# Kernel tuning notes

Measured on AMD Instinct MI355X. Metric: run time of the kernel, lower is better.

Reference implementation:

```python
import jax, jax.numpy as jnp
import numpy as np

B, S, E, H = 4, 2048, 1024, 16
D = E // H


def setup_inputs() -> dict:
    key = jax.random.key(0)
    ks = jax.random.split(key, 4)
    scale = 0.02
    x = jax.random.normal(ks[0], (B, S, E), dtype=jnp.float32)
    in_proj_w = jax.random.normal(ks[1], (3 * E, E), dtype=jnp.float32) * scale
    in_proj_b = jnp.zeros((3 * E,), dtype=jnp.float32)
    out_w = jax.random.normal(ks[2], (E, E), dtype=jnp.float32) * scale
    out_b = jnp.zeros((E,), dtype=jnp.float32)
    rel_bias = jax.random.normal(ks[3], (2 * 32 + 1, H), dtype=jnp.float32) * 0.02
    return {"x": x, "in_proj_w": in_proj_w, "in_proj_b": in_proj_b,
            "out_w": out_w, "out_b": out_b, "rel_bias": rel_bias,
            "max_rel_dist": 32}


def reference(x, in_proj_w, in_proj_b, out_w, out_b, rel_bias, max_rel_dist):
    b, s, e = x.shape
    h = rel_bias.shape[1]
    d = e // h
    # relative-position indices, clamped: [S, S]
    i = jnp.arange(s)[:, None]
    j = jnp.arange(s)[None, :]
    rel = jnp.clip(i - j, -max_rel_dist, max_rel_dist) + max_rel_dist
    # gather per-pair per-head bias then average over heads -> single 2D mask
    attn_mask = jnp.mean(rel_bias[rel], axis=-1)  # [S, S]
    # fused QKV projection (PyTorch in_proj: x @ W^T + b)
    qkv = x @ in_proj_w.T + in_proj_b           # [B, S, 3E]
    q, k, v = jnp.split(qkv, 3, axis=-1)
    q = q.reshape(b, s, h, d)
    k = k.reshape(b, s, h, d)
    v = v.reshape(b, s, h, d)
    scale = 1.0 / jnp.sqrt(jnp.asarray(d, dtype=x.dtype))
    scores = jnp.einsum('bqhd,bkhd->bhqk', q, k) * scale + attn_mask  # [B,H,S,S]
    probs = jax.nn.softmax(scores, axis=-1)
    ctx = jnp.einsum('bhqk,bkhd->bqhd', probs, v).reshape(b, s, e)
    return ctx @ out_w.T + out_b
```

## Files before the change

kernel.cpp:

```cpp
#include <hip/hip_runtime.h>
#include <math.h>

#define B_ 4
#define S_ 2048
#define E_ 1024
#define H_ 16
#define D_ 64
#define MRD 32

typedef __bf16 bf16x8 __attribute__((ext_vector_type(8)));
typedef float f32x4 __attribute__((ext_vector_type(4)));
typedef unsigned short us8 __attribute__((ext_vector_type(8)));
typedef unsigned short us4 __attribute__((ext_vector_type(4)));

union frag_cvt { us8 u; bf16x8 b; };
union h_cvt { __bf16 h; unsigned short u; };

__device__ __forceinline__ unsigned short bhi(float x) {
    h_cvt c; c.h = (__bf16)x; return c.u;
}
__device__ __forceinline__ float bf16_f(unsigned short h) {
    union { unsigned int u; float f; } c;
    c.u = ((unsigned int)h) << 16;
    return c.f;
}

__device__ __forceinline__ void async_copy16(const void* g, void* l) {
    __builtin_amdgcn_global_load_lds(
        (const __attribute__((address_space(1))) void*)g,
        (__attribute__((address_space(3))) void*)l,
        16, 0, 0);
}

__device__ __forceinline__ f32x4 mf16(const frag_cvt& a, const frag_cvt& b, f32x4 c) {
    return __builtin_amdgcn_mfma_f32_16x16x32_bf16(a.b, b.b, c, 0, 0, 0);
}

#define QSCL 0.18033688f
#define L2E  1.44269504f

#define SBAR0() __builtin_amdgcn_sched_barrier(0)

__global__ __launch_bounds__(128) void cvt_bf16(
    const float* __restrict__ in, unsigned short* __restrict__ out, int K)
{
    const int r  = blockIdx.x;
    const int k8 = threadIdx.x * 8;
    if (k8 >= K) return;
    const float* p = in + (size_t)r * K + k8;
    float4 a = *(const float4*)p;
    float4 b = *(const float4*)(p + 4);
    float xs[8] = {a.x, a.y, a.z, a.w, b.x, b.y, b.z, b.w};
    us8 hu;
#pragma unroll
    for (int j = 0; j < 8; ++j) hu[j] = bhi(xs[j]);
    *(us8*)&out[(size_t)r * K + k8] = hu;
}

__global__ __launch_bounds__(128) void split_hilo(
    const float* __restrict__ in, unsigned short* __restrict__ out, int K)
{
    const int r  = blockIdx.x;
    const int k8 = threadIdx.x * 8;
    if (k8 >= K) return;
    const float* p = in + (size_t)r * K + k8;
    float4 a = *(const float4*)p;
    float4 b = *(const float4*)(p + 4);
    float xs[8] = {a.x, a.y, a.z, a.w, b.x, b.y, b.z, b.w};
    us8 hu, lu;
#pragma unroll
    for (int j = 0; j < 8; ++j) {
        unsigned short hb = bhi(xs[j]);
        hu[j] = hb;
        lu[j] = bhi(xs[j] - bf16_f(hb));
    }
    *(us8*)&out[(size_t)r * 2 * K + k8]     = hu;
    *(us8*)&out[(size_t)r * 2 * K + K + k8] = lu;
}

__device__ __forceinline__ void stage_unit(const unsigned short* g, int grs,
                                           unsigned short* lu, int t)
{
#pragma unroll
    for (int l = 0; l < 2; ++l) {
        const int f  = l * 512 + t;
        const int ri = f >> 3;
        const int cs = ((f & 7) ^ (ri & 7)) * 8;
        async_copy16(g + (size_t)ri * grs + cs,
                     lu + l * 4096 + (t >> 6) * 512);
    }
}

template<int MODE>
__global__ __launch_bounds__(512, 2) void gemm8(
    const unsigned short* __restrict__ Ag, const unsigned short* __restrict__ Bg,
    const float* __restrict__ bias,
    unsigned short* __restrict__ O0, unsigned short* __restrict__ O1,
    unsigned short* __restrict__ O2, float* __restrict__ Cf)
{
    constexpr int KD = (MODE == 0) ? 1024 : 3072;
    constexpr int NT = KD / 64;
    constexpr int AS = (MODE == 0) ? 1024 : 2048;
    constexpr int BS = (MODE == 0) ? 1024 : 2048;

    __shared__ unsigned short sbuf[2][24576];

    const int t    = threadIdx.x;
    const int lane = t & 63;
    const int w    = t >> 6;
    const int ln   = lane & 15;
    const int quad = lane >> 4;
    const int wm   = w >> 1;
    const int wn   = w & 1;
    const int m0   = blockIdx.x * 256;
    const int n0   = blockIdx.y * 128;

    auto mapA = [](int kk) -> int {
        return (MODE == 0) ? kk : (kk < 1024 ? kk : kk - 1024);
    };
    auto mapB = [](int kk) -> int {
        return (MODE == 0) ? kk : (kk < 2048 ? kk : kk - 2048);
    };

    const int swz = (ln & 7) << 3;
    const int kq0 = (quad * 8) ^ swz;
    const int kq1 = (32 + quad * 8) ^ swz;

    f32x4 acc[4][4];
#pragma unroll
    for (int i = 0; i < 4; ++i)
#pragma unroll
        for (int j = 0; j < 4; ++j)
            acc[i][j] = (f32x4){0.f, 0.f, 0.f, 0.f};

    stage_unit(Ag + (size_t)m0 * AS + mapA(0),         AS, &sbuf[0][0],     t);
    stage_unit(Ag + (size_t)(m0 + 128) * AS + mapA(0), AS, &sbuf[0][8192],  t);
    stage_unit(Bg + (size_t)n0 * BS + mapB(0),         BS, &sbuf[0][16384], t);
    stage_unit(Bg + (size_t)n0 * BS + mapB(64),        BS, &sbuf[1][16384], t);
    stage_unit(Ag + (size_t)m0 * AS + mapA(64),        AS, &sbuf[1][0],     t);
    asm volatile("s_waitcnt vmcnt(4)" ::: "memory");
    SBAR0();
    __builtin_amdgcn_s_barrier();
    SBAR0();

    for (int k = 0; k < NT; ++k) {
        unsigned short* bufc = sbuf[k & 1];
        unsigned short* bufn = sbuf[(k & 1) ^ 1];
        frag_cvt a0[2][2], a1[2][2], b0[2][2], b1[2][2];

#pragma unroll
        for (int i = 0; i < 2; ++i) {
            const int ra = (wm * 64 + i * 16 + ln) * 64;
            a0[i][0].u = *(const us8*)&bufc[ra + kq0];
            a0[i][1].u = *(const us8*)&bufc[ra + kq1];
            const int rb = 16384 + (wn * 64 + i * 16 + ln) * 64;
            b0[i][0].u = *(const us8*)&bufc[rb + kq0];
            b0[i][1].u = *(const us8*)&bufc[rb + kq1];
        }
        if (k + 1 < NT)
            stage_unit(Ag + (size_t)(m0 + 128) * AS + mapA((k + 1) * 64),
                       AS, &bufn[8192], t);
        SBAR0(); __builtin_amdgcn_s_barrier(); SBAR0();
        __builtin_amdgcn_s_setprio(1);
#pragma unroll
        for (int i = 0; i < 2; ++i)
#pragma unroll
            for (int j = 0; j < 2; ++j) {
                acc[i][j] = mf16(a0[i][0], b0[j][0], acc[i][j]);
                acc[i][j] = mf16(a0[i][1], b0[j][1], acc[i][j]);
            }
        __builtin_amdgcn_s_setprio(0);
        SBAR0(); __builtin_amdgcn_s_barrier(); SBAR0();

#pragma unroll
        for (int i = 0; i < 2; ++i) {
            const int rb = 16384 + (wn * 64 + (i + 2) * 16 + ln) * 64;
            b1[i][0].u = *(const us8*)&bufc[rb + kq0];
            b1[i][1].u = *(const us8*)&bufc[rb + kq1];
        }
        SBAR0(); __builtin_amdgcn_s_barrier(); SBAR0();
        __builtin_amdgcn_s_setprio(1);
#pragma unroll
        for (int i = 0; i < 2; ++i)
#pragma unroll
            for (int j = 0; j < 2; ++j) {
                acc[i][j + 2] = mf16(a0[i][0], b1[j][0], acc[i][j + 2]);
                acc[i][j + 2] = mf16(a0[i][1], b1[j][1], acc[i][j + 2]);
            }
        __builtin_amdgcn_s_setprio(0);
        SBAR0(); __builtin_amdgcn_s_barrier(); SBAR0();

#pragma unroll
        for (int i = 0; i < 2; ++i) {
            const int ra = (wm * 64 + (i + 2) * 16 + ln) * 64;
            a1[i][0].u = *(const us8*)&bufc[ra + kq0];
            a1[i][1].u = *(const us8*)&bufc[ra + kq1];
        }
        if (k + 2 < NT)
            stage_unit(Bg + (size_t)n0 * BS + mapB((k + 2) * 64),
                       BS, &bufc[16384], t);
        SBAR0(); __builtin_amdgcn_s_barrier(); SBAR0();
        __builtin_amdgcn_s_setprio(1);
#pragma unroll
        for (int i = 0; i < 2; ++i)
#pragma unroll
            for (int j = 0; j < 2; ++j) {
                acc[i + 2][j + 2] = mf16(a1[i][0], b1[j][0], acc[i + 2][j + 2]);
                acc[i + 2][j + 2] = mf16(a1[i][1], b1[j][1], acc[i + 2][j + 2]);
            }
        __builtin_amdgcn_s_setprio(0);
        SBAR0(); __builtin_amdgcn_s_barrier(); SBAR0();

        if (k + 2 < NT)
            stage_unit(Ag + (size_t)m0 * AS + mapA((k + 2) * 64),
                       AS, &bufc[0], t);
        SBAR0(); __builtin_amdgcn_s_barrier(); SBAR0();
        __builtin_amdgcn_s_setprio(1);
#pragma unroll
        for (int i = 0; i < 2; ++i)
#pragma unroll
            for (int j = 0; j < 2; ++j) {
                acc[i + 2][j] = mf16(a1[i][0], b0[j][0], acc[i + 2][j]);
                acc[i + 2][j] = mf16(a1[i][1], b0[j][1], acc[i + 2][j]);
            }
        __builtin_amdgcn_s_setprio(0);
        if (k + 2 < NT) {
            asm volatile("s_waitcnt vmcnt(4)" ::: "memory");
        } else if (k + 1 < NT) {
            asm volatile("s_waitcnt vmcnt(0)" ::: "memory");
        }
        SBAR0(); __builtin_amdgcn_s_barrier(); SBAR0();
    }

    if constexpr (MODE == 0) {
        if (n0 < E_) {
#pragma unroll
            for (int j = 0; j < 4; ++j) {
                const int col = n0 + wn * 64 + j * 16 + ln;
                const float bv = bias[col];
                const int h = (col & (E_ - 1)) >> 6, d = col & 63;
#pragma unroll
                for (int i = 0; i < 4; ++i) {
#pragma unroll
                    for (int r = 0; r < 4; ++r) {
                        const int row = m0 + wm * 64 + i * 16 + quad * 4 + r;
                        const int b = row >> 11, s = row & (S_ - 1);
                        O0[((size_t)(b * 16 + h) * S_ + s) * 64 + d] =
                            bhi((acc[i][j][r] + bv) * QSCL);
                    }
                }
            }
        } else if (n0 < 2 * E_) {
#pragma unroll
            for (int j = 0; j < 4; ++j) {
                const int col = n0 + wn * 64 + j * 16 + ln;
                const float bv = bias[col];
                const int h = (col & (E_ - 1)) >> 6, d = col & 63;
#pragma unroll
                for (int i = 0; i < 4; ++i) {
#pragma unroll
                    for (int r = 0; r < 4; ++r) {
                        const int row = m0 + wm * 64 + i * 16 + quad * 4 + r;
                        const int b = row >> 11, s = row & (S_ - 1);
                        O1[((size_t)(b * 16 + h) * S_ + s) * 64 +
                           (((d >> 3) ^ (s & 7)) * 8) + (d & 7)] =
                            bhi(acc[i][j][r] + bv);
                    }
                }
            }
        } else {
#pragma unroll
            for (int j = 0; j < 4; ++j) {
                const int col = n0 + wn * 64 + j * 16 + ln;
                const float bv = bias[col];
                const int h = (col & (E_ - 1)) >> 6, d = col & 63;
#pragma unroll
                for (int i = 0; i < 4; ++i) {
                    const int row0 = m0 + wm * 64 + i * 16 + quad * 4;
                    const int b = row0 >> 11, s0 = row0 & (S_ - 1);
                    const int tile = s0 >> 6;
                    const int g = (s0 >> 3) & 7;
                    us4 o;
#pragma unroll
                    for (int r = 0; r < 4; ++r) o[r] = bhi(acc[i][j][r] + bv);
                    *(us4*)&O2[(size_t)(b * 16 + h) * S_ * 64 + tile * 4096 +
                               d * 64 + ((g ^ (d & 7)) * 8) + (quad & 1) * 4] = o;
                }
            }
        }
    } else {
#pragma unroll
        for (int j = 0; j < 4; ++j) {
            const int col = n0 + wn * 64 + j * 16 + ln;
            const float bv = bias[col];
#pragma unroll
            for (int i = 0; i < 4; ++i) {
                const int row = m0 + wm * 64 + i * 16 + quad * 4;
#pragma unroll
                for (int r = 0; r < 4; ++r)
                    Cf[(size_t)(row + r) * E_ + col] = acc[i][j][r] + bv;
            }
        }
    }
}

__global__ __launch_bounds__(256, 4) void attn_mfma5(
    const unsigned short* __restrict__ Qb, const unsigned short* __restrict__ K2,
    const unsigned short* __restrict__ Vt2, const float* __restrict__ rel_bias,
    unsigned short* __restrict__ ctx2)
{
    __shared__ unsigned short Kt[64 * 64];
    __shared__ unsigned short Vt[64 * 64];
    __shared__ unsigned short Pt[128 * 72];
    __shared__ float bias_s[65];

    const int t    = threadIdx.x;
    const int w    = t >> 6;
    const int lane = t & 63;
    const int ln   = lane & 15;
    const int quad = lane >> 4;

    const int bh = blockIdx.x;
    const int b  = bh >> 4;
    const int h  = bh & 15;
    const int q0 = blockIdx.y * 128;

    if (t < 65) {
        float s = 0.f;
#pragma unroll
        for (int hh = 0; hh < 16; ++hh) s += rel_bias[t * 16 + hh];
        bias_s[t] = s * (L2E / 16.f);
    }

    frag_cvt qf[2][2];
#pragma unroll
    for (int mf = 0; mf < 2; ++mf) {
        const unsigned short* qp =
            Qb + ((size_t)bh * S_ + q0 + w * 32 + mf * 16 + ln) * 64;
        qf[mf][0].u = *(const us8*)(qp + quad * 8);
        qf[mf][1].u = *(const us8*)(qp + 32 + quad * 8);
    }

    frag_cvt ones;
#pragma unroll
    for (int j = 0; j < 8; ++j) ones.u[j] = 0x3F80;

    f32x4 O[2][4];
#pragma unroll
    for (int mf = 0; mf < 2; ++mf)
#pragma unroll
        for (int n = 0; n < 4; ++n) O[mf][n] = (f32x4){0.f, 0.f, 0.f, 0.f};
    f32x4 lacc[2] = {(f32x4){0.f, 0.f, 0.f, 0.f}, (f32x4){0.f, 0.f, 0.f, 0.f}};

    const unsigned short* Kg = K2  + (size_t)bh * S_ * 64;
    const unsigned short* Vg = Vt2 + (size_t)bh * S_ * 64;

    for (int k0 = 0; k0 < S_; k0 += 64) {
        __syncthreads();
        {
            const unsigned short* kg = Kg + (size_t)k0 * 64;
            const unsigned short* vg = Vg + (size_t)k0 * 64;
            const int uo = w * 512;
            async_copy16(kg + uo + lane * 8,        &Kt[uo]);
            async_copy16(kg + 2048 + uo + lane * 8, &Kt[2048 + uo]);
            async_copy16(vg + uo + lane * 8,        &Vt[uo]);
            async_copy16(vg + 2048 + uo + lane * 8, &Vt[2048 + uo]);
        }
        __syncthreads();

        f32x4 sa[2][4];
#pragma unroll
        for (int n = 0; n < 4; ++n) {
            sa[0][n] = (f32x4){0.f, 0.f, 0.f, 0.f};
            sa[1][n] = (f32x4){0.f, 0.f, 0.f, 0.f};
            const int ro = (n * 16 + ln) * 64;
#pragma unroll
            for (int ks = 0; ks < 2; ++ks) {
                frag_cvt kh;
                kh.u = *(const us8*)&Kt[ro + (((ks * 4 + quad) ^ (ln & 7)) * 8)];
                sa[0][n] = __builtin_amdgcn_mfma_f32_16x16x32_bf16(
                    qf[0][ks].b, kh.b, sa[0][n], 0, 0, 0);
                sa[1][n] = __builtin_amdgcn_mfma_f32_16x16x32_bf16(
                    qf[1][ks].b, kh.b, sa[1][n], 0, 0, 0);
            }
        }

        const bool inband = (k0 >= q0 - 64) && (k0 <= q0 + 128);
        float cb = 0.f;
        if (!inband) cb = bias_s[(k0 < q0) ? 64 : 0];
#pragma unroll
        for (int mf = 0; mf < 2; ++mf) {
#pragma unroll
            for (int n = 0; n < 4; ++n) {
#pragma unroll
                for (int r = 0; r < 4; ++r) {
                    float s2;
                    if (inband) {
                        const int q   = q0 + w * 32 + mf * 16 + quad * 4 + r;
                        const int key = k0 + n * 16 + ln;
                        int rel = q - key;
                        rel = (rel < -MRD) ? -MRD : (rel > MRD ? MRD : rel);
                        s2 = sa[mf][n][r] + bias_s[rel + MRD];
                    } else {
                        s2 = sa[mf][n][r] + cb;
                    }
                    const int qrow = w * 32 + mf * 16 + quad * 4 + r;
                    const int pos = (n * 16 + ln) ^ ((qrow & 8) << 1);
                    Pt[qrow * 72 + pos] = bhi(__builtin_amdgcn_exp2f(s2));
                }
            }
        }

#pragma unroll
        for (int ks = 0; ks < 2; ++ks) {
            frag_cvt pa[2];
#pragma unroll
            for (int mf = 0; mf < 2; ++mf) {
                const int prow = w * 32 + mf * 16 + ln;
                pa[mf].u = *(const us8*)&Pt[prow * 72 +
                           ((ks * 32 + quad * 8) ^ ((prow & 8) << 1))];
                lacc[mf] = __builtin_amdgcn_mfma_f32_16x16x32_bf16(
                    pa[mf].b, ones.b, lacc[mf], 0, 0, 0);
            }
#pragma unroll
            for (int n = 0; n < 4; ++n) {
                frag_cvt vh;
                vh.u = *(const us8*)&Vt[(n * 16 + ln) * 64 +
                                        (((ks * 4 + quad) ^ (ln & 7)) * 8)];
                O[0][n] = __builtin_amdgcn_mfma_f32_16x16x32_bf16(
                    pa[0].b, vh.b, O[0][n], 0, 0, 0);
                O[1][n] = __builtin_amdgcn_mfma_f32_16x16x32_bf16(
                    pa[1].b, vh.b, O[1][n], 0, 0, 0);
            }
        }
    }

#pragma unroll
    for (int mf = 0; mf < 2; ++mf) {
        float inv[4];
#pragma unroll
        for (int r = 0; r < 4; ++r) inv[r] = 1.f / lacc[mf][r];
#pragma unroll
        for (int n = 0; n < 4; ++n) {
            const int k = h * D_ + n * 16 + ln;
#pragma unroll
            for (int r = 0; r < 4; ++r) {
                const int q = q0 + w * 32 + mf * 16 + quad * 4 + r;
                const float v = O[mf][n][r] * inv[r];
                unsigned short hb = bhi(v);
                const size_t rb = (size_t)(b * S_ + q) * (2 * E_);
                ctx2[rb + k]      = hb;
                ctx2[rb + E_ + k] = bhi(v - bf16_f(hb));
            }
        }
    }
}

extern "C" void kernel_launch(void* const* d_in, const int* in_sizes, int n_in,
                              void* d_out, int out_size, void* d_ws, size_t ws_size,
                              hipStream_t stream)
{
    const float* x         = (const float*)d_in[0];
    const float* in_proj_w = (const float*)d_in[1];
    const float* in_proj_b = (const float*)d_in[2];
    const float* out_w     = (const float*)d_in[3];
    const float* out_b     = (const float*)d_in[4];
    const float* rel_bias  = (const float*)d_in[5];
    float* out = (float*)d_out;

    const int M = B_ * S_;
    const size_t PH = (size_t)B_ * H_ * S_ * 64;

    unsigned short* Qb   = (unsigned short*)d_ws;
    unsigned short* K2   = Qb + PH;
    unsigned short* Vt2  = K2 + PH;
    unsigned short* W2o  = Vt2 + PH;
    unsigned short* Wqkv = W2o + (size_t)E_ * 2 * E_;
    unsigned short* A2c  = Wqkv + (size_t)3 * E_ * E_;
    unsigned short* Axb  = A2c;

    cvt_bf16<<<M,      128, 0, stream>>>(x,         Axb,  E_);
    cvt_bf16<<<3 * E_, 128, 0, stream>>>(in_proj_w, Wqkv, E_);

    {
        dim3 grid(M / 256, (3 * E_) / 128);
        gemm8<0><<<grid, 512, 0, stream>>>(Axb, Wqkv, in_proj_b,
                                           Qb, K2, Vt2, nullptr);
    }
    {
        dim3 grid(B_ * H_, S_ / 128);
        attn_mfma5<<<grid, 256, 0, stream>>>(Qb, K2, Vt2, rel_bias, A2c);
    }
    split_hilo<<<E_, 128, 0, stream>>>(out_w, W2o, E_);
    {
        dim3 grid(M / 256, E_ / 128);
        gemm8<1><<<grid, 512, 0, stream>>>(A2c, W2o, out_b,
                                           nullptr, nullptr, nullptr, out);
    }
}
```

Before: 332.3 us.

## Simplify GEMM main loop to single load-then-compute phase per k-tile

Replaces the four-phase interleaved GEMM loop, which used many barriers, sched_barriers and staggered per-unit async stages, with a simpler schedule. Each k-step now loads all A/B fragments from LDS, runs all 32 MFMAs, then issues the full next-next tile prefetch between two barriers. This cuts barrier count and scheduling constraints, but loses fine-grained overlap of the LDS reads and global loads with MFMA work, and raises register pressure from holding all fragments at once.

```diff
diff --git a/kernel.cpp b/kernel.cpp
--- a/kernel.cpp
+++ b/kernel.cpp
@@ -38,8 +38,6 @@
 
 #define QSCL 0.18033688f
 #define L2E  1.44269504f
-
-#define SBAR0() __builtin_amdgcn_sched_barrier(0)
 
 __global__ __launch_bounds__(128) void cvt_bf16(
     const float* __restrict__ in, unsigned short* __restrict__ out, int K)
@@ -133,103 +131,53 @@
         for (int j = 0; j < 4; ++j)
             acc[i][j] = (f32x4){0.f, 0.f, 0.f, 0.f};
 
-    stage_unit(Ag + (size_t)m0 * AS + mapA(0),         AS, &sbuf[0][0],     t);
-    stage_unit(Ag + (size_t)(m0 + 128) * AS + mapA(0), AS, &sbuf[0][8192],  t);
-    stage_unit(Bg + (size_t)n0 * BS + mapB(0),         BS, &sbuf[0][16384], t);
-    stage_unit(Bg + (size_t)n0 * BS + mapB(64),        BS, &sbuf[1][16384], t);
-    stage_unit(Ag + (size_t)m0 * AS + mapA(64),        AS, &sbuf[1][0],     t);
-    asm volatile("s_waitcnt vmcnt(4)" ::: "memory");
-    SBAR0();
+    stage_unit(Ag + (size_t)m0 * AS + mapA(0),          AS, &sbuf[0][0],     t);
+    stage_unit(Ag + (size_t)(m0 + 128) * AS + mapA(0),  AS, &sbuf[0][8192],  t);
+    stage_unit(Bg + (size_t)n0 * BS + mapB(0),          BS, &sbuf[0][16384], t);
+    stage_unit(Ag + (size_t)m0 * AS + mapA(64),         AS, &sbuf[1][0],     t);
+    stage_unit(Ag + (size_t)(m0 + 128) * AS + mapA(64), AS, &sbuf[1][8192],  t);
+    stage_unit(Bg + (size_t)n0 * BS + mapB(64),         BS, &sbuf[1][16384], t);
+    asm volatile("s_waitcnt vmcnt(6)" ::: "memory");
     __builtin_amdgcn_s_barrier();
-    SBAR0();
 
     for (int k = 0; k < NT; ++k) {
         unsigned short* bufc = sbuf[k & 1];
-        unsigned short* bufn = sbuf[(k & 1) ^ 1];
-        frag_cvt a0[2][2], a1[2][2], b0[2][2], b1[2][2];
-
-#pragma unroll
-        for (int i = 0; i < 2; ++i) {
+        frag_cvt af[4][2], bg[4][2];
+
+#pragma unroll
+        for (int i = 0; i < 4; ++i) {
             const int ra = (wm * 64 + i * 16 + ln) * 64;
-            a0[i][0].u = *(const us8*)&bufc[ra + kq0];
-            a0[i][1].u = *(const us8*)&bufc[ra + kq1];
+            af[i][0].u = *(const us8*)&bufc[ra + kq0];
+            af[i][1].u = *(const us8*)&bufc[ra + kq1];
             const int rb = 16384 + (wn * 64 + i * 16 + ln) * 64;
-            b0[i][0].u = *(const us8*)&bufc[rb + kq0];
-            b0[i][1].u = *(const us8*)&bufc[rb + kq1];
-        }
-        if (k + 1 < NT)
-            stage_unit(Ag + (size_t)(m0 + 128) * AS + mapA((k + 1) * 64),
-                       AS, &bufn[8192], t);
-        SBAR0(); __builtin_amdgcn_s_barrier(); SBAR0();
+            bg[i][0].u = *(const us8*)&bufc[rb + kq0];
+            bg[i][1].u = *(const us8*)&bufc[rb + kq1];
+        }
         __builtin_amdgcn_s_setprio(1);
 #pragma unroll
-        for (int i = 0; i < 2; ++i)
-#pragma unroll
-            for (int j = 0; j < 2; ++j) {
-                acc[i][j] = mf16(a0[i][0], b0[j][0], acc[i][j]);
-                acc[i][j] = mf16(a0[i][1], b0[j][1], acc[i][j]);
+        for (int i = 0; i < 4; ++i)
+#pragma unroll
+            for (int j = 0; j < 4; ++j) {
+                acc[i][j] = mf16(af[i][0], bg[j][0], acc[i][j]);
+                acc[i][j] = mf16(af[i][1], bg[j][1], acc[i][j]);
             }
         __builtin_amdgcn_s_setprio(0);
-        SBAR0(); __builtin_amdgcn_s_barrier(); SBAR0();
-
-#pragma unroll
-        for (int i = 0; i < 2; ++i) {
-            const int rb = 16384 + (wn * 64 + (i + 2) * 16 + ln) * 64;
-            b1[i][0].u = *(const us8*)&bufc[rb + kq0];
-            b1[i][1].u = *(const us8*)&bufc[rb + kq1];
-        }
-        SBAR0(); __builtin_amdgcn_s_barrier(); SBAR0();
-        __builtin_amdgcn_s_setprio(1);
-#pragma unroll
-        for (int i = 0; i < 2; ++i)
-#pragma unroll
-            for (int j = 0; j < 2; ++j) {
-                acc[i][j + 2] = mf16(a0[i][0], b1[j][0], acc[i][j + 2]);
-                acc[i][j + 2] = mf16(a0[i][1], b1[j][1], acc[i][j + 2]);
-            }
-        __builtin_amdgcn_s_setprio(0);
-        SBAR0(); __builtin_amdgcn_s_barrier(); SBAR0();
-
-#pragma unroll
-        for (int i = 0; i < 2; ++i) {
-            const int ra = (wm * 64 + (i + 2) * 16 + ln) * 64;
-            a1[i][0].u = *(const us8*)&bufc[ra + kq0];
-            a1[i][1].u = *(const us8*)&bufc[ra + kq1];
-        }
-        if (k + 2 < NT)
-            stage_unit(Bg + (size_t)n0 * BS + mapB((k + 2) * 64),
-                       BS, &bufc[16384], t);
-        SBAR0(); __builtin_amdgcn_s_barrier(); SBAR0();
-        __builtin_amdgcn_s_setprio(1);
-#pragma unroll
-        for (int i = 0; i < 2; ++i)
-#pragma unroll
-            for (int j = 0; j < 2; ++j) {
-                acc[i + 2][j + 2] = mf16(a1[i][0], b1[j][0], acc[i + 2][j + 2]);
-                acc[i + 2][j + 2] = mf16(a1[i][1], b1[j][1], acc[i + 2][j + 2]);
-            }
-        __builtin_amdgcn_s_setprio(0);
-        SBAR0(); __builtin_amdgcn_s_barrier(); SBAR0();
-
-        if (k + 2 < NT)
-            stage_unit(Ag + (size_t)m0 * AS + mapA((k + 2) * 64),
-                       AS, &bufc[0], t);
-        SBAR0(); __builtin_amdgcn_s_barrier(); SBAR0();
-        __builtin_amdgcn_s_setprio(1);
-#pragma unroll
-        for (int i = 0; i < 2; ++i)
-#pragma unroll
-            for (int j = 0; j < 2; ++j) {
-                acc[i + 2][j] = mf16(a1[i][0], b0[j][0], acc[i + 2][j]);
-                acc[i + 2][j] = mf16(a1[i][1], b0[j][1], acc[i + 2][j]);
-            }
-        __builtin_amdgcn_s_setprio(0);
+
+        if (k == NT - 1) break;
+
+        __builtin_amdgcn_s_barrier();
+
         if (k + 2 < NT) {
-            asm volatile("s_waitcnt vmcnt(4)" ::: "memory");
-        } else if (k + 1 < NT) {
+            const int kk = (k + 2) * 64;
+            stage_unit(Ag + (size_t)m0 * AS + mapA(kk),         AS, &bufc[0],     t);
+            stage_unit(Ag + (size_t)(m0 + 128) * AS + mapA(kk), AS, &bufc[8192],  t);
+            stage_unit(Bg + (size_t)n0 * BS + mapB(kk),         BS, &bufc[16384], t);
+            asm volatile("s_waitcnt vmcnt(6)" ::: "memory");
+        } else {
             asm volatile("s_waitcnt vmcnt(0)" ::: "memory");
         }
-        SBAR0(); __builtin_amdgcn_s_barrier(); SBAR0();
+
+        __builtin_amdgcn_s_barrier();
     }
 
     if constexpr (MODE == 0) {
```

Measured after the change: 326.0 us. About the same (-1.9%).
